# Kernel optimization log

Hardware: AMD Instinct MI355X
Metric: run time of the kernel (lower is better)

The kernel has to match this reference:

```python
import math
import jax, jax.numpy as jnp
import numpy as np

B, S, D_MODEL = 4, 2048, 1024
N_HEADS, D_KV = 16, 64
INNER = N_HEADS * D_KV
NUM_BUCKETS = 32
MAX_DISTANCE = 128


def _relative_position_bucket(relative_position, bidirectional=True,
                              num_buckets=32, max_distance=128):
    # Faithful port of T5Attention._relative_position_bucket
    ret = jnp.zeros_like(relative_position)
    n = -relative_position
    if bidirectional:
        num_buckets //= 2
        ret = ret + (n < 0).astype(jnp.int32) * num_buckets
        n = jnp.abs(n)
    else:
        n = jnp.maximum(n, 0)
    max_exact = num_buckets // 2
    is_small = n < max_exact
    # safe log: n>=max_exact wherever this branch is selected
    val_if_large = max_exact + (
        jnp.log(jnp.maximum(n, 1).astype(jnp.float32) / max_exact)
        / math.log(max_distance / max_exact) * (num_buckets - max_exact)
    ).astype(jnp.int32)
    val_if_large = jnp.minimum(val_if_large, num_buckets - 1)
    return ret + jnp.where(is_small, n, val_if_large)


def setup_inputs() -> dict:
    key = jax.random.key(0)
    k_h, k_q, k_k, k_v, k_o, k_e = jax.random.split(key, 6)
    std = D_MODEL ** -0.5
    return {
        "hidden_states": jax.random.normal(k_h, (B, S, D_MODEL), dtype=jnp.float32),
        "Wq": jax.random.normal(k_q, (D_MODEL, INNER), dtype=jnp.float32) * std,
        "Wk": jax.random.normal(k_k, (D_MODEL, INNER), dtype=jnp.float32) * std,
        "Wv": jax.random.normal(k_v, (D_MODEL, INNER), dtype=jnp.float32) * std,
        "Wo": jax.random.normal(k_o, (INNER, D_MODEL), dtype=jnp.float32) * std,
        "rel_emb": jax.random.normal(k_e, (NUM_BUCKETS, N_HEADS), dtype=jnp.float32) * std,
    }


def reference(hidden_states, Wq, Wk, Wv, Wo, rel_emb):
    b, s, _ = hidden_states.shape
    # QKV projections (T5: no bias, no 1/sqrt(d) scaling of scores)
    def shape_heads(x):  # [b, s, inner] -> [b, h, s, d_kv]
        return x.reshape(b, s, N_HEADS, D_KV).transpose(0, 2, 1, 3)
    q = shape_heads(hidden_states @ Wq)
    k = shape_heads(hidden_states @ Wk)
    v = shape_heads(hidden_states @ Wv)

    scores = jnp.einsum("bhqd,bhkd->bhqk", q, k)  # [b, h, s, s]

    # relative position bias: sequential_relative_position + bucket + embed
    context_pos = jnp.arange(s, dtype=jnp.int32)[:, None]
    memory_pos = jnp.arange(s, dtype=jnp.int32)[None, :]
    rel_pos = memory_pos - context_pos  # [s, s]
    rp_bucket = _relative_position_bucket(rel_pos, bidirectional=True,
                                          num_buckets=NUM_BUCKETS,
                                          max_distance=MAX_DISTANCE)
    bias = rel_emb[rp_bucket]                       # [s, s, h]
    bias = bias.transpose(2, 0, 1)[None]            # [1, h, s, s]

    weights = jax.nn.softmax(scores + bias, axis=-1)
    context = jnp.einsum("bhqk,bhkd->bhqd", weights, v)
    context = context.transpose(0, 2, 1, 3).reshape(b, s, INNER)
    return context @ Wo
```

## Files before the change

kernel.cpp:

```cpp
#include <hip/hip_runtime.h>

typedef __bf16 bf16_t;
typedef __bf16 bf16x4 __attribute__((ext_vector_type(4)));
typedef __bf16 bf16x8 __attribute__((ext_vector_type(8)));
typedef float f32x4 __attribute__((ext_vector_type(4)));

#define NB 4
#define SS 2048
#define DM 1024
#define NH 16
#define DK 64
#define MM (NB*SS)
#define LOG2E 1.44269504f

__global__ __launch_bounds__(256) void k_prep(
    const float* __restrict__ H, bf16_t* __restrict__ Hbf,
    const float* __restrict__ W0, const float* __restrict__ W1,
    const float* __restrict__ W2, const float* __restrict__ W3,
    bf16_t* __restrict__ T0, bf16_t* __restrict__ T1,
    bf16_t* __restrict__ T2, bf16_t* __restrict__ T3,
    const float* __restrict__ rel_emb, float* __restrict__ biasT) {
  __shared__ float t[64][65];
  const int blk = blockIdx.x, tid = threadIdx.x;
  if (blk < 8192) {
    int i = blk * 256 + tid;
    float4 v = ((const float4*)H)[i];
    bf16x4 o = {(bf16_t)v.x, (bf16_t)v.y, (bf16_t)v.z, (bf16_t)v.w};
    *(bf16x4*)(Hbf + 4 * (size_t)i) = o;
  } else if (blk < 9216) {
    int tt = blk - 8192;
    int which = tt >> 8, rem = tt & 255;
    int k0 = (rem >> 4) * 64, n0 = (rem & 15) * 64;
    const float* W = which == 0 ? W0 : which == 1 ? W1 : which == 2 ? W2 : W3;
    bf16_t* T = which == 0 ? T0 : which == 1 ? T1 : which == 2 ? T2 : T3;
#pragma unroll
    for (int i = 0; i < 16; i++) {
      int idx = tid + i * 256; int r = idx >> 6, c = idx & 63;
      t[r][c] = W[(size_t)(k0 + r) * DM + n0 + c];
    }
    __syncthreads();
#pragma unroll
    for (int i = 0; i < 16; i++) {
      int idx = tid + i * 256; int r = idx >> 6, c = idx & 63;
      T[(size_t)(n0 + r) * DM + k0 + c] = (bf16_t)t[c][r];
    }
  } else {
    int tt = (blk - 9216) * 256 + tid;
    if (tt < 2 * SS - 1) {
      int rel = tt - (SS - 1);
      int n = -rel;
      int ret = 0;
      if (n < 0) { ret = 16; n = -n; }
      int bucket;
      if (n < 8) bucket = n;
      else {
        int v = 8 + (int)(logf((float)n * 0.125f) * (8.0f / logf(16.0f)));
        bucket = v < 15 ? v : 15;
      }
      bucket += ret;
#pragma unroll
      for (int h = 0; h < NH; h++)
        biasT[h * (2 * SS - 1) + tt] = rel_emb[bucket * NH + h] * LOG2E;
    }
  }
}

__device__ __forceinline__ void gld16(const bf16_t* g, bf16_t* l) {
  __builtin_amdgcn_global_load_lds(
      (const __attribute__((address_space(1))) unsigned int*)g,
      (__attribute__((address_space(3))) unsigned int*)l, 16, 0, 0);
}

__device__ __forceinline__ void gemm_tile(const bf16_t* __restrict__ A,
                                          const bf16_t* __restrict__ Bt, const int K,
                                          const int m0, const int n0,
                                          bf16_t* As, bf16_t* Bs, f32x4 (&acc)[4][4]) {
  const int tid = threadIdx.x;
  const int lane = tid & 63, wave = tid >> 6;
  const int l15 = lane & 15, quad = lane >> 4;
  const int wm = (wave >> 1) * 64, wn = (wave & 1) * 64;
  const int wwu = __builtin_amdgcn_readfirstlane(wave);
  const f32x4 z4 = {0.f, 0.f, 0.f, 0.f};
#pragma unroll
  for (int i = 0; i < 4; i++)
#pragma unroll
    for (int j = 0; j < 4; j++) acc[i][j] = z4;

  const int rr = lane >> 2;
  const int cc = (lane & 3) * 8;
  for (int k0 = 0; k0 < K; k0 += 32) {
    __syncthreads();
    gld16(A + (size_t)(m0 + wwu * 32 + rr) * K + k0 + cc,       As + wwu * 1024);
    gld16(A + (size_t)(m0 + wwu * 32 + 16 + rr) * K + k0 + cc,  As + wwu * 1024 + 512);
    gld16(Bt + (size_t)(n0 + wwu * 32 + rr) * K + k0 + cc,      Bs + wwu * 1024);
    gld16(Bt + (size_t)(n0 + wwu * 32 + 16 + rr) * K + k0 + cc, Bs + wwu * 1024 + 512);
    __syncthreads();
    bf16x8 af[4], bfr[4];
#pragma unroll
    for (int i = 0; i < 4; i++) {
      af[i]  = *(const bf16x8*)(As + (wm + i * 16 + l15) * 32 + quad * 8);
      bfr[i] = *(const bf16x8*)(Bs + (wn + i * 16 + l15) * 32 + quad * 8);
    }
#pragma unroll
    for (int i = 0; i < 4; i++)
#pragma unroll
      for (int j = 0; j < 4; j++)
        acc[i][j] = __builtin_amdgcn_mfma_f32_16x16x32_bf16(af[i], bfr[j], acc[i][j], 0, 0, 0);
  }
}

__global__ __launch_bounds__(256) void k_gemm_qkv(
    const bf16_t* __restrict__ A, const bf16_t* __restrict__ Wqt,
    const bf16_t* __restrict__ Wkt, const bf16_t* __restrict__ Wvt,
    bf16_t* __restrict__ Q, bf16_t* __restrict__ Kf, bf16_t* __restrict__ Vf) {
  __shared__ bf16_t As[128 * 32];
  __shared__ bf16_t Bs[128 * 32];
  const int which = blockIdx.z;
  const bf16_t* Bt = which == 0 ? Wqt : (which == 1 ? Wkt : Wvt);
  const int m0 = blockIdx.x * 128, n0 = blockIdx.y * 128;
  f32x4 acc[4][4];
  gemm_tile(A, Bt, DM, m0, n0, As, Bs, acc);

  const int tid = threadIdx.x;
  const int lane = tid & 63, wave = tid >> 6;
  const int l15 = lane & 15, quad = lane >> 4;
  const int wm = (wave >> 1) * 64, wn = (wave & 1) * 64;

  if (which == 0) {
#pragma unroll
    for (int i = 0; i < 4; i++)
#pragma unroll
      for (int j = 0; j < 4; j++)
#pragma unroll
        for (int r = 0; r < 4; r++) {
          int m = m0 + wm + i * 16 + quad * 4 + r;
          int n = n0 + wn + j * 16 + l15;
          int b = m >> 11, s = m & (SS - 1);
          int h = n >> 6, d = n & 63;
          Q[(((size_t)(b * NH + h)) * SS + s) * DK + d] = (bf16_t)(acc[i][j][r] * LOG2E);
        }
  } else if (which == 1) {
#pragma unroll
    for (int i = 0; i < 4; i++)
#pragma unroll
      for (int j = 0; j < 4; j++)
#pragma unroll
        for (int r = 0; r < 4; r++) {
          int m = m0 + wm + i * 16 + quad * 4 + r;
          int n = n0 + wn + j * 16 + l15;
          int b = m >> 11, s = m & (SS - 1);
          int h = n >> 6, d = n & 63;
          int slot = 4 * ((s >> 5) & 1) + 2 * ((s >> 2) & 1) + (d >> 5);
          int fl = ((d >> 3) & 3) * 16 + 4 * ((s >> 3) & 3) + (s & 3);
          Kf[(((size_t)(b * NH + h) * 32 + (s >> 6)) * 8 + slot) * 512 + fl * 8 + (d & 7)] =
              (bf16_t)acc[i][j][r];
        }
  } else {
#pragma unroll
    for (int i = 0; i < 4; i++)
#pragma unroll
      for (int j = 0; j < 4; j++) {
        int m = m0 + wm + i * 16 + quad * 4;
        int n = n0 + wn + j * 16 + l15;
        int b = m >> 11, s = m & (SS - 1);
        int h = n >> 6, d = n & 63;
        int slot = 4 * ((s >> 5) & 1) + (d >> 4);
        int fl = ((s >> 3) & 3) * 16 + (d & 15);
        bf16x4 pk = {(bf16_t)acc[i][j][0], (bf16_t)acc[i][j][1],
                     (bf16_t)acc[i][j][2], (bf16_t)acc[i][j][3]};
        *(bf16x4*)(&Vf[(((size_t)(b * NH + h) * 32 + (s >> 6)) * 8 + slot) * 512 +
                       fl * 8 + (s & 7)]) = pk;
      }
  }
}

__global__ __launch_bounds__(256, 3) void k_attn(const bf16_t* __restrict__ Qg,
                                                 const bf16_t* __restrict__ Kf,
                                                 const bf16_t* __restrict__ Vf,
                                                 const float* __restrict__ biasT,
                                                 bf16_t* __restrict__ ctx) {
  const int lin = blockIdx.x + 16 * blockIdx.y;
  const int nid = (lin & 7) * 128 + (lin >> 3);
  const int bh = nid >> 4;
  const int it0 = (nid & 15) * 128;
  const int b = bh >> 4, h = bh & 15;
  const bf16_t* Qp = Qg + ((size_t)bh * SS + it0) * DK;
  const float* biasH = biasT + h * (2 * SS - 1);

  __shared__ float bias2[512][2];
  __shared__ float OsumS[2][4][16];
  __shared__ f32x4 Ored[2 * 4 * 4 * 64];

  const int tid = threadIdx.x;
  const int lane = tid & 63, wave = tid >> 6;
  const int l15 = lane & 15, quad = lane >> 4;
  const int kh = wave & 1, qh = wave >> 1;

  for (int w = tid; w < 512; w += 256) {
    int g = w - 256 + (SS - 1);
    bias2[w][0] = biasH[g];
    bias2[w][1] = biasH[g + 1];
  }
  const float Bpos = biasH[(SS - 1) + 1024];
  const float Bneg = biasH[(SS - 1) - 1024];

  const bf16_t* KfB = Kf + (size_t)bh * 32 * 4096 + lane * 8;
  const bf16_t* VfB = Vf + (size_t)bh * 32 * 4096 + lane * 8;
  auto loadfrag = [&](int it, bf16x8 (&kf)[2][2], bf16x8 (&vf)[4]) {
    const bf16_t* kb = KfB + (size_t)it * 4096;
#pragma unroll
    for (int t = 0; t < 2; t++)
#pragma unroll
      for (int hf = 0; hf < 2; hf++)
        kf[t][hf] = *(const bf16x8*)(kb + ((2 * kh + t) * 2 + hf) * 512);
    const bf16_t* vb = VfB + (size_t)it * 4096;
#pragma unroll
    for (int ni = 0; ni < 4; ni++)
      vf[ni] = *(const bf16x8*)(vb + (kh * 4 + ni) * 512);
  };

  bf16x8 qf[4][2];
#pragma unroll
  for (int mi = 0; mi < 4; mi++) {
    const bf16_t* qr = Qp + (size_t)(64 * qh + mi * 16 + l15) * DK + quad * 8;
    qf[mi][0] = *(const bf16x8*)qr;
    qf[mi][1] = *(const bf16x8*)(qr + 32);
  }

  f32x4 accO[4][4], accS[4];
  const f32x4 z4 = {0.f, 0.f, 0.f, 0.f};
#pragma unroll
  for (int mi = 0; mi < 4; mi++) {
    accS[mi] = z4;
#pragma unroll
    for (int ni = 0; ni < 4; ni++) accO[mi][ni] = z4;
  }
  const bf16_t one = (bf16_t)1.0f;
  const bf16x8 ones = {one, one, one, one, one, one, one, one};

  const int wb0 = 32 * kh + 8 * quad - 64 * qh - l15 - it0 + 256;

  auto body = [&](int it, bf16x8 (&kf)[2][2], bf16x8 (&vf)[4]) {
    const int diff = it * 64 - it0;
    const bool band = (diff >= -128) && (diff < 256);
    const float cconst = diff >= 256 ? Bpos : Bneg;
    const f32x4 csplat = {cconst, cconst, cconst, cconst};
    const int jb = it * 64 + wb0;
#pragma unroll
    for (int mi = 0; mi < 4; mi++) {
      f32x4 c0, c1;
      if (band) {
        const int w = jb - mi * 16;
        float2 a0 = *(const float2*)bias2[w],     b0 = *(const float2*)bias2[w + 2];
        float2 a1 = *(const float2*)bias2[w + 4], b1 = *(const float2*)bias2[w + 6];
        c0 = f32x4{a0.x, a0.y, b0.x, b0.y};
        c1 = f32x4{a1.x, a1.y, b1.x, b1.y};
      } else {
        c0 = csplat;
        c1 = csplat;
      }
      f32x4 s0 = __builtin_amdgcn_mfma_f32_16x16x32_bf16(
          kf[0][1], qf[mi][1],
          __builtin_amdgcn_mfma_f32_16x16x32_bf16(kf[0][0], qf[mi][0], c0, 0, 0, 0), 0, 0, 0);
      f32x4 s1 = __builtin_amdgcn_mfma_f32_16x16x32_bf16(
          kf[1][1], qf[mi][1],
          __builtin_amdgcn_mfma_f32_16x16x32_bf16(kf[1][0], qf[mi][0], c1, 0, 0, 0), 0, 0, 0);
      bf16x8 pf = {(bf16_t)__builtin_amdgcn_exp2f(s0[0]), (bf16_t)__builtin_amdgcn_exp2f(s0[1]),
                   (bf16_t)__builtin_amdgcn_exp2f(s0[2]), (bf16_t)__builtin_amdgcn_exp2f(s0[3]),
                   (bf16_t)__builtin_amdgcn_exp2f(s1[0]), (bf16_t)__builtin_amdgcn_exp2f(s1[1]),
                   (bf16_t)__builtin_amdgcn_exp2f(s1[2]), (bf16_t)__builtin_amdgcn_exp2f(s1[3])};
#pragma unroll
      for (int ni = 0; ni < 4; ni++)
        accO[mi][ni] = __builtin_amdgcn_mfma_f32_16x16x32_bf16(vf[ni], pf, accO[mi][ni], 0, 0, 0);
      accS[mi] = __builtin_amdgcn_mfma_f32_16x16x32_bf16(ones, pf, accS[mi], 0, 0, 0);
    }
  };

  bf16x8 kf[2][2], vf[4];
  loadfrag(0, kf, vf);
  __syncthreads();

  for (int it = 0; it < 31; ++it) {
    body(it, kf, vf);
    loadfrag(it + 1, kf, vf);
  }
  body(31, kf, vf);

  __syncthreads();
  if (kh) {
#pragma unroll
    for (int mi = 0; mi < 4; mi++) {
#pragma unroll
      for (int ni = 0; ni < 4; ni++)
        Ored[((qh * 4 + mi) * 4 + ni) * 64 + lane] = accO[mi][ni];
      if (quad == 0) OsumS[qh][mi][l15] = accS[mi][0];
    }
  }
  __syncthreads();
  if (!kh) {
#pragma unroll
    for (int mi = 0; mi < 4; mi++) {
      float l = accS[mi][0] + OsumS[qh][mi][l15];
      float inv = 1.0f / l;
      int srow = it0 + 64 * qh + mi * 16 + l15;
#pragma unroll
      for (int ni = 0; ni < 4; ni++) {
        f32x4 o = accO[mi][ni] + Ored[((qh * 4 + mi) * 4 + ni) * 64 + lane];
        bf16x4 pk = {(bf16_t)(o[0] * inv), (bf16_t)(o[1] * inv),
                     (bf16_t)(o[2] * inv), (bf16_t)(o[3] * inv)};
        *(bf16x4*)(&ctx[((size_t)(b * SS + srow)) * DM + h * DK + ni * 16 + quad * 4]) = pk;
      }
    }
  }
}

__global__ __launch_bounds__(256) void k_gemm_out(const bf16_t* __restrict__ A,
                                                  const bf16_t* __restrict__ Wot,
                                                  float* __restrict__ out) {
  __shared__ bf16_t As[128 * 32];
  __shared__ bf16_t Bs[128 * 32];
  const int m0 = blockIdx.x * 128, n0 = blockIdx.y * 128;
  f32x4 acc[4][4];
  gemm_tile(A, Wot, DM, m0, n0, As, Bs, acc);

  const int tid = threadIdx.x;
  const int lane = tid & 63, wave = tid >> 6;
  const int l15 = lane & 15, quad = lane >> 4;
  const int wm = (wave >> 1) * 64, wn = (wave & 1) * 64;
#pragma unroll
  for (int i = 0; i < 4; i++)
#pragma unroll
    for (int j = 0; j < 4; j++)
#pragma unroll
      for (int r = 0; r < 4; r++) {
        int m = m0 + wm + i * 16 + quad * 4 + r;
        int n = n0 + wn + j * 16 + l15;
        out[(size_t)m * DM + n] = acc[i][j][r];
      }
}

extern "C" void kernel_launch(void* const* d_in, const int* in_sizes, int n_in,
                              void* d_out, int out_size, void* d_ws, size_t ws_size,
                              hipStream_t stream) {
  (void)in_sizes; (void)n_in; (void)out_size; (void)ws_size;
  const float* H  = (const float*)d_in[0];
  const float* Wq = (const float*)d_in[1];
  const float* Wk = (const float*)d_in[2];
  const float* Wv = (const float*)d_in[3];
  const float* Wo = (const float*)d_in[4];
  const float* rel = (const float*)d_in[5];
  float* out = (float*)d_out;

  char* w = (char*)d_ws;
  bf16_t* Hbf = (bf16_t*)w; w += (size_t)MM * DM * 2;
  bf16_t* Wqt = (bf16_t*)w; w += (size_t)DM * DM * 2;
  bf16_t* Wkt = (bf16_t*)w; w += (size_t)DM * DM * 2;
  bf16_t* Wvt = (bf16_t*)w; w += (size_t)DM * DM * 2;
  bf16_t* Wot = (bf16_t*)w; w += (size_t)DM * DM * 2;
  bf16_t* Q   = (bf16_t*)w; w += (size_t)MM * DM * 2;
  bf16_t* Kf  = (bf16_t*)w; w += (size_t)MM * DM * 2;
  bf16_t* Vf  = (bf16_t*)w; w += (size_t)MM * DM * 2;
  bf16_t* CTX = (bf16_t*)w; w += (size_t)MM * DM * 2;
  float* biasT = (float*)w;

  k_prep<<<9232, 256, 0, stream>>>(H, Hbf, Wq, Wk, Wv, Wo, Wqt, Wkt, Wvt, Wot, rel, biasT);
  k_gemm_qkv<<<dim3(MM / 128, DM / 128, 3), 256, 0, stream>>>(Hbf, Wqt, Wkt, Wvt, Q, Kf, Vf);
  k_attn<<<dim3(SS / 128, NB * NH), 256, 0, stream>>>(Q, Kf, Vf, biasT, CTX);
  k_gemm_out<<<dim3(MM / 128, DM / 128), 256, 0, stream>>>(CTX, Wot, out);
}
```

Baseline: 266.4 us.

## Software-pipeline attention loop: overlap PV MFMAs of previous tile with QK of current

```diff
diff --git a/kernel.cpp b/kernel.cpp
--- a/kernel.cpp
+++ b/kernel.cpp
@@ -174,7 +174,7 @@
   }
 }
 
-__global__ __launch_bounds__(256, 3) void k_attn(const bf16_t* __restrict__ Qg,
+__global__ __launch_bounds__(256, 2) void k_attn(const bf16_t* __restrict__ Qg,
                                                  const bf16_t* __restrict__ Kf,
                                                  const bf16_t* __restrict__ Vf,
                                                  const float* __restrict__ biasT,
@@ -206,13 +206,15 @@
 
   const bf16_t* KfB = Kf + (size_t)bh * 32 * 4096 + lane * 8;
   const bf16_t* VfB = Vf + (size_t)bh * 32 * 4096 + lane * 8;
-  auto loadfrag = [&](int it, bf16x8 (&kf)[2][2], bf16x8 (&vf)[4]) {
+  auto loadK = [&](int it, bf16x8 (&kf)[2][2]) {
     const bf16_t* kb = KfB + (size_t)it * 4096;
 #pragma unroll
     for (int t = 0; t < 2; t++)
 #pragma unroll
       for (int hf = 0; hf < 2; hf++)
         kf[t][hf] = *(const bf16x8*)(kb + ((2 * kh + t) * 2 + hf) * 512);
+  };
+  auto loadV = [&](int it, bf16x8 (&vf)[4]) {
     const bf16_t* vb = VfB + (size_t)it * 4096;
 #pragma unroll
     for (int ni = 0; ni < 4; ni++)
@@ -240,7 +242,8 @@
 
   const int wb0 = 32 * kh + 8 * quad - 64 * qh - l15 - it0 + 256;
 
-  auto body = [&](int it, bf16x8 (&kf)[2][2], bf16x8 (&vf)[4]) {
+  auto step = [&](int it, bf16x8 (&kfC)[2][2], bf16x8 (&pfP)[4], bf16x8 (&vfP)[4],
+                  bf16x8 (&pfC)[4]) {
     const int diff = it * 64 - it0;
     const bool band = (diff >= -128) && (diff < 256);
     const float cconst = diff >= 256 ? Bpos : Bneg;
@@ -260,31 +263,82 @@
         c1 = csplat;
       }
       f32x4 s0 = __builtin_amdgcn_mfma_f32_16x16x32_bf16(
-          kf[0][1], qf[mi][1],
-          __builtin_amdgcn_mfma_f32_16x16x32_bf16(kf[0][0], qf[mi][0], c0, 0, 0, 0), 0, 0, 0);
+          kfC[0][1], qf[mi][1],
+          __builtin_amdgcn_mfma_f32_16x16x32_bf16(kfC[0][0], qf[mi][0], c0, 0, 0, 0), 0, 0, 0);
       f32x4 s1 = __builtin_amdgcn_mfma_f32_16x16x32_bf16(
-          kf[1][1], qf[mi][1],
-          __builtin_amdgcn_mfma_f32_16x16x32_bf16(kf[1][0], qf[mi][0], c1, 0, 0, 0), 0, 0, 0);
-      bf16x8 pf = {(bf16_t)__builtin_amdgcn_exp2f(s0[0]), (bf16_t)__builtin_amdgcn_exp2f(s0[1]),
-                   (bf16_t)__builtin_amdgcn_exp2f(s0[2]), (bf16_t)__builtin_amdgcn_exp2f(s0[3]),
-                   (bf16_t)__builtin_amdgcn_exp2f(s1[0]), (bf16_t)__builtin_amdgcn_exp2f(s1[1]),
-                   (bf16_t)__builtin_amdgcn_exp2f(s1[2]), (bf16_t)__builtin_amdgcn_exp2f(s1[3])};
+          kfC[1][1], qf[mi][1],
+          __builtin_amdgcn_mfma_f32_16x16x32_bf16(kfC[1][0], qf[mi][0], c1, 0, 0, 0), 0, 0, 0);
 #pragma unroll
       for (int ni = 0; ni < 4; ni++)
-        accO[mi][ni] = __builtin_amdgcn_mfma_f32_16x16x32_bf16(vf[ni], pf, accO[mi][ni], 0, 0, 0);
-      accS[mi] = __builtin_amdgcn_mfma_f32_16x16x32_bf16(ones, pf, accS[mi], 0, 0, 0);
+        accO[mi][ni] =
+            __builtin_amdgcn_mfma_f32_16x16x32_bf16(vfP[ni], pfP[mi], accO[mi][ni], 0, 0, 0);
+      accS[mi] = __builtin_amdgcn_mfma_f32_16x16x32_bf16(ones, pfP[mi], accS[mi], 0, 0, 0);
+      pfC[mi] =
+          bf16x8{(bf16_t)__builtin_amdgcn_exp2f(s0[0]), (bf16_t)__builtin_amdgcn_exp2f(s0[1]),
+                 (bf16_t)__builtin_amdgcn_exp2f(s0[2]), (bf16_t)__builtin_amdgcn_exp2f(s0[3]),
+                 (bf16_t)__builtin_amdgcn_exp2f(s1[0]), (bf16_t)__builtin_amdgcn_exp2f(s1[1]),
+                 (bf16_t)__builtin_amdgcn_exp2f(s1[2]), (bf16_t)__builtin_amdgcn_exp2f(s1[3])};
     }
   };
-
-  bf16x8 kf[2][2], vf[4];
-  loadfrag(0, kf, vf);
+  auto step0 = [&](bf16x8 (&kfC)[2][2], bf16x8 (&pfC)[4]) {
+    const int diff = -it0;
+    const bool band = (diff >= -128) && (diff < 256);
+    const float cconst = diff >= 256 ? Bpos : Bneg;
+    const f32x4 csplat = {cconst, cconst, cconst, cconst};
+    const int jb = wb0;
+#pragma unroll
+    for (int mi = 0; mi < 4; mi++) {
+      f32x4 c0, c1;
+      if (band) {
+        const int w = jb - mi * 16;
+        float2 a0 = *(const float2*)bias2[w],     b0 = *(const float2*)bias2[w + 2];
+        float2 a1 = *(const float2*)bias2[w + 4], b1 = *(const float2*)bias2[w + 6];
+        c0 = f32x4{a0.x, a0.y, b0.x, b0.y};
+        c1 = f32x4{a1.x, a1.y, b1.x, b1.y};
+      } else {
+        c0 = csplat;
+        c1 = csplat;
+      }
+      f32x4 s0 = __builtin_amdgcn_mfma_f32_16x16x32_bf16(
+          kfC[0][1], qf[mi][1],
+          __builtin_amdgcn_mfma_f32_16x16x32_bf16(kfC[0][0], qf[mi][0], c0, 0, 0, 0), 0, 0, 0);
+      f32x4 s1 = __builtin_amdgcn_mfma_f32_16x16x32_bf16(
+          kfC[1][1], qf[mi][1],
+          __builtin_amdgcn_mfma_f32_16x16x32_bf16(kfC[1][0], qf[mi][0], c1, 0, 0, 0), 0, 0, 0);
+      pfC[mi] =
+          bf16x8{(bf16_t)__builtin_amdgcn_exp2f(s0[0]), (bf16_t)__builtin_amdgcn_exp2f(s0[1]),
+                 (bf16_t)__builtin_amdgcn_exp2f(s0[2]), (bf16_t)__builtin_amdgcn_exp2f(s0[3]),
+                 (bf16_t)__builtin_amdgcn_exp2f(s1[0]), (bf16_t)__builtin_amdgcn_exp2f(s1[1]),
+                 (bf16_t)__builtin_amdgcn_exp2f(s1[2]), (bf16_t)__builtin_amdgcn_exp2f(s1[3])};
+    }
+  };
+
+  bf16x8 kfA[2][2], vfA[4], kfB[2][2], vfB[4], pfA[4], pfB[4];
+  loadK(0, kfA);
+  loadV(0, vfA);
   __syncthreads();
-
-  for (int it = 0; it < 31; ++it) {
-    body(it, kf, vf);
-    loadfrag(it + 1, kf, vf);
-  }
-  body(31, kf, vf);
+  loadK(1, kfB);
+  step0(kfA, pfA);
+  loadV(1, vfB);
+
+  for (int it = 1; it < 32; it += 2) {
+    if (it + 1 < 32) loadK(it + 1, kfA);
+    step(it, kfB, pfA, vfA, pfB);
+    if (it + 1 < 32) {
+      loadV(it + 1, vfA);
+      loadK(it + 2, kfB);
+      step(it + 1, kfA, pfB, vfB, pfA);
+      loadV(it + 2, vfB);
+    }
+  }
+#pragma unroll
+  for (int mi = 0; mi < 4; mi++) {
+#pragma unroll
+    for (int ni = 0; ni < 4; ni++)
+      accO[mi][ni] =
+          __builtin_amdgcn_mfma_f32_16x16x32_bf16(vfB[ni], pfB[mi], accO[mi][ni], 0, 0, 0);
+    accS[mi] = __builtin_amdgcn_mfma_f32_16x16x32_bf16(ones, pfB[mi], accS[mi], 0, 0, 0);
+  }
 
   __syncthreads();
   if (kh) {
```

Result: faster. 260.7 us (median of 2 runs) (-2.1%).
